# Kernel tuning notes

Measured on AMD Instinct MI355X. Metric: run time of the kernel, lower is better.

## Reference

```python
import jax, jax.numpy as jnp
import numpy as np

N, E, E3, DIM = 25000, 50000, 40000, 64


def setup_inputs() -> dict:
    key = jax.random.key(0)
    ks = jax.random.split(key, 16)
    def g(k, shape, scale=0.1):
        return jax.random.normal(k, shape, jnp.float32) * scale
    return {
        "x": jax.random.normal(ks[0], (N, 8), jnp.float32),
        "edge_attr": jax.random.uniform(ks[1], (E, 19), dtype=jnp.float32),
        "edge_attr3": jax.random.uniform(ks[2], (E3, 8), dtype=jnp.float32),
        "edge_index": jax.random.randint(ks[3], (2, E), 0, N),
        "edge_index3": jax.random.randint(ks[4], (2, E3), 0, N),
        "W_node": g(ks[5], (8, DIM)), "b_node": jnp.zeros((DIM,), jnp.float32),
        "W_ea": g(ks[6], (19, 12)), "b_ea": jnp.zeros((12,), jnp.float32),
        "W_e1": g(ks[7], (12, 128)), "b_e1": jnp.zeros((128,), jnp.float32),
        "W_e2": g(ks[8], (128, DIM * DIM), 0.01), "b_e2": jnp.zeros((DIM * DIM,), jnp.float32),
        "conv_bias": jnp.zeros((DIM,), jnp.float32),
        "W_ih": g(ks[9], (3 * DIM, DIM)), "b_ih": jnp.zeros((3 * DIM,), jnp.float32),
        "W_hh": g(ks[10], (3 * DIM, DIM)), "b_hh": jnp.zeros((3 * DIM,), jnp.float32),
        "W_l1": g(ks[11], (DIM + 8, 128)), "b_l1": jnp.zeros((128,), jnp.float32),
        "W_l2": g(ks[12], (128, 1)), "b_l2": jnp.zeros((1,), jnp.float32),
    }


def _forward(x, edge_attr, edge_attr3,
             W_node, b_node, W_ea, b_ea, W_e1, b_e1, W_e2, b_e2, conv_bias,
             W_ih, b_ih, W_hh, b_hh, W_l1, b_l1, W_l2, b_l2,
             edge_index, edge_index3):
    dim = W_node.shape[1]
    n = x.shape[0]
    out = jax.nn.relu(x @ W_node + b_node)                      # [N, dim]
    ea = jax.nn.relu(edge_attr @ W_ea + b_ea)                   # [E, 12]
    # edge MLP -> per-edge dim x dim weight matrices (same for all 3 conv calls)
    Wedge = (jax.nn.relu(ea @ W_e1 + b_e1) @ W_e2 + b_e2).reshape(-1, dim, dim)  # [E, dim, dim]
    src, dst = edge_index[0], edge_index[1]
    ones = jnp.ones((src.shape[0],), x.dtype)
    cnt = jnp.maximum(jax.ops.segment_sum(ones, dst, num_segments=n), 1.0)  # [N]
    h = out
    for _ in range(3):
        msg = jnp.einsum('ed,edf->ef', out[src], Wedge)                     # per-edge GEMV
        agg = jax.ops.segment_sum(msg, dst, num_segments=n) / cnt[:, None]  # scatter-mean
        m = jax.nn.relu(agg + conv_bias)
        # single-step GRU (PyTorch gate order: r, z, n)
        gi = m @ W_ih.T + b_ih
        gh = h @ W_hh.T + b_hh
        ir, iz, inn = jnp.split(gi, 3, axis=-1)
        hr, hz, hn = jnp.split(gh, 3, axis=-1)
        r = jax.nn.sigmoid(ir + hr)
        z = jax.nn.sigmoid(iz + hz)
        ng = jnp.tanh(inn + r * hn)
        h = (1.0 - z) * ng + z * h
        out = h
    pair = (out[edge_index3[0]] + out[edge_index3[1]]) * 0.5    # mean over the 2 endpoints
    yhat = jnp.concatenate([pair, edge_attr3], axis=1)          # [E3, dim+8]
    yhat = jax.nn.relu(yhat @ W_l1 + b_l1) @ W_l2 + b_l2        # [E3, 1]
    return yhat[:, 0]


def reference(x, edge_attr, edge_attr3, edge_index, edge_index3,
              W_node, b_node, W_ea, b_ea, W_e1, b_e1, W_e2, b_e2, conv_bias,
              W_ih, b_ih, W_hh, b_hh, W_l1, b_l1, W_l2, b_l2):
    return _forward(x, edge_attr, edge_attr3,
                    W_node, b_node, W_ea, b_ea, W_e1, b_e1, W_e2, b_e2, conv_bias,
                    W_ih, b_ih, W_hh, b_hh, W_l1, b_l1, W_l2, b_l2,
                    edge_index, edge_index3)
```

## Files before the change

### kernel.cpp

```cpp
#include <hip/hip_runtime.h>

typedef unsigned short u16;
typedef unsigned int u32;
typedef __attribute__((ext_vector_type(8))) short short8v;
typedef __attribute__((ext_vector_type(4))) float float4v;

__device__ __forceinline__ float sigm(float x) { return 1.0f / (1.0f + __expf(-x)); }
__device__ __forceinline__ u16 f2bf(float f) {
  u32 u = __float_as_uint(f);
  u32 r = (u + 0x7fffu + ((u >> 16) & 1u)) >> 16;
  return (u16)r;
}
__device__ __forceinline__ float bf2f(u16 w) { return __uint_as_float(((u32)w) << 16); }

__global__ void k_zero_f(float* __restrict__ p, int n) {
  int i = blockIdx.x * blockDim.x + threadIdx.x;
  if (i < n) p[i] = 0.0f;
}
__global__ void k_zero_i(int* __restrict__ p, int n) {
  int i = blockIdx.x * blockDim.x + threadIdx.x;
  if (i < n) p[i] = 0;
}

__global__ void k_cnt(const int* __restrict__ dst, int* __restrict__ cnt, int E) {
  int e = blockIdx.x * blockDim.x + threadIdx.x;
  if (e < E) atomicAdd(&cnt[dst[e]], 1);
}

__global__ void k_node(const float* __restrict__ x, const float* __restrict__ Wn,
                       const float* __restrict__ bn, float* __restrict__ h, int N) {
  int tid = blockIdx.x * blockDim.x + threadIdx.x;
  if (tid >= N * 64) return;
  int n = tid >> 6, f = tid & 63;
  float acc = bn[f];
  for (int k = 0; k < 8; ++k) acc += x[(size_t)n * 8 + k] * Wn[k * 64 + f];
  h[tid] = fmaxf(acc, 0.0f);
}

__global__ __launch_bounds__(256) void k_edge_mlp(
    const float* __restrict__ ea_in, const float* __restrict__ Wea,
    const float* __restrict__ bea, const float* __restrict__ We1,
    const float* __restrict__ be1, u16* __restrict__ Ahi, int E) {
  __shared__ float att[2][19];
  __shared__ float ea[2][12];
  int half = threadIdx.x >> 7;
  int t = threadIdx.x & 127;
  int e = blockIdx.x * 2 + half;
  bool real = (e < E);
  int ee = real ? e : E - 1;
  if (t < 19) att[half][t] = ea_in[(size_t)ee * 19 + t];
  __syncthreads();
  if (t < 12) {
    float a = bea[t];
#pragma unroll
    for (int k = 0; k < 19; ++k) a += att[half][k] * Wea[k * 12 + t];
    ea[half][t] = fmaxf(a, 0.0f);
  }
  __syncthreads();
  float a = be1[t];
#pragma unroll
  for (int j = 0; j < 12; ++j) a += ea[half][j] * We1[j * 128 + t];
  if (real) Ahi[(size_t)e * 128 + t] = f2bf(fmaxf(a, 0.0f));
}

__global__ void k_pack_b(const float* __restrict__ W2, u16* __restrict__ Bph) {
  int tid = blockIdx.x * blockDim.x + threadIdx.x;
  if (tid >= 128 * 4096) return;
  int j = tid & 7;
  int lane = (tid >> 3) & 63;
  int nt = (tid >> 9) & 3;
  int ks = (tid >> 11) & 3;
  int d = tid >> 13;
  int c = lane & 15, q = lane >> 4;
  int k = ks * 32 + q * 8 + j;
  int n = d * 64 + nt * 16 + c;
  Bph[tid] = f2bf(W2[(size_t)k * 4096 + n]);
}

__global__ void k_prep_wtf(const float* __restrict__ Wih, const float* __restrict__ Whh,
                           u16* __restrict__ WpI, u16* __restrict__ WpH) {
  int tid = blockIdx.x * blockDim.x + threadIdx.x;
  if (tid >= 2 * 12288) return;
  int w = tid / 12288;
  int r = tid - w * 12288;
  int jj = r & 7;
  int lane = (r >> 3) & 63;
  int t = r >> 9;
  int nt = t % 12, ks = t / 12;
  int c = lane & 15, q = lane >> 4;
  int j = nt * 16 + c;
  int k = ks * 32 + q * 8 + jj;
  const float* W = w ? Whh : Wih;
  u16* Wp = w ? WpH : WpI;
  Wp[r] = f2bf(W[j * 64 + k]);
}

__global__ void k_prep_wl1(const float* __restrict__ Wl1, u16* __restrict__ Wp1) {
  int tid = blockIdx.x * blockDim.x + threadIdx.x;
  if (tid >= 3 * 8 * 64 * 8) return;
  int j = tid & 7;
  int lane = (tid >> 3) & 63;
  int nt = (tid >> 9) & 7;
  int ks = tid >> 12;
  int c = lane & 15, q = lane >> 4;
  int k = ks * 32 + q * 8 + j;
  int n = nt * 16 + c;
  Wp1[tid] = f2bf((k < 72) ? Wl1[k * 128 + n] : 0.0f);
}

__global__ __launch_bounds__(256, 2) void k_conv_fused(
    const u16* __restrict__ Ahi, const u16* __restrict__ Bph,
    const float* __restrict__ b2, const float* __restrict__ h,
    const int* __restrict__ src, const int* __restrict__ dst,
    float* __restrict__ agg, int E) {
  __shared__ __align__(16) u16 sAh[128 * 136];
  __shared__ __align__(16) float hs[128 * 36];
  __shared__ __align__(16) float sb2[2048];
  int m0 = blockIdx.x * 128;
  int d0 = blockIdx.y * 32;
  int tid = threadIdx.x;
#pragma unroll
  for (int p = 0; p < 8; ++p) {
    int slot = p * 256 + tid;
    int r = slot >> 4, s = slot & 15;
    int gr = m0 + r;
    if (gr >= E) gr = E - 1;
    *(uint4*)(&sAh[r * 136 + s * 8]) = *(const uint4*)(Ahi + (size_t)gr * 128 + s * 8);
  }
#pragma unroll
  for (int p = 0; p < 4; ++p) {
    int slot = p * 256 + tid;
    int r = slot >> 3, s = slot & 7;
    int ge = m0 + r;
    if (ge >= E) ge = E - 1;
    int sn = src[ge];
    *(float4*)(&hs[r * 36 + s * 4]) = *(const float4*)(h + (size_t)sn * 64 + d0 + s * 4);
  }
#pragma unroll
  for (int p = 0; p < 2; ++p) {
    int slot = p * 256 + tid;
    *(float4*)(&sb2[slot * 4]) = *(const float4*)(b2 + d0 * 64 + slot * 4);
  }
  __syncthreads();
  int wave = tid >> 6, lane = tid & 63;
  int c = lane & 15, q = lane >> 4;
  float msg[2][4][4];
#pragma unroll
  for (int mt = 0; mt < 2; ++mt)
#pragma unroll
    for (int nt = 0; nt < 4; ++nt)
#pragma unroll
      for (int r = 0; r < 4; ++r) msg[mt][nt][r] = 0.0f;

  short8v bufA[16], bufB[16];
  auto loadB = [&](int dd, short8v* buf) {
    const u16* bp = Bph + (size_t)dd * 8192 + lane * 8;
#pragma unroll
    for (int i = 0; i < 16; ++i) buf[i] = *(const short8v*)(bp + i * 512);
  };
  auto compute = [&](int dd, const short8v* buf) {
    int dl = dd - d0;
#pragma unroll
    for (int mt = 0; mt < 2; ++mt) {
      int arow = wave * 32 + mt * 16 + c;
      float4v acc[4];
#pragma unroll
      for (int nt = 0; nt < 4; ++nt) acc[nt] = (float4v){0.f, 0.f, 0.f, 0.f};
#pragma unroll
      for (int ks = 0; ks < 4; ++ks) {
        short8v ah = *(const short8v*)(&sAh[arow * 136 + ks * 32 + q * 8]);
#pragma unroll
        for (int nt = 0; nt < 4; ++nt)
          acc[nt] = __builtin_amdgcn_mfma_f32_16x16x32_bf16(ah, buf[ks * 4 + nt], acc[nt], 0, 0, 0);
      }
      float hd[4];
#pragma unroll
      for (int r = 0; r < 4; ++r)
        hd[r] = hs[(wave * 32 + mt * 16 + q * 4 + r) * 36 + dl];
#pragma unroll
      for (int nt = 0; nt < 4; ++nt) {
        float b2v = sb2[dl * 64 + nt * 16 + c];
#pragma unroll
        for (int r = 0; r < 4; ++r) msg[mt][nt][r] += hd[r] * (acc[nt][r] + b2v);
      }
    }
  };

  loadB(d0, bufA);
  for (int d = d0; d < d0 + 32; d += 2) {
    loadB(d + 1, bufB);
    compute(d, bufA);
    if (d + 2 < d0 + 32) loadB(d + 2, bufA);
    compute(d + 1, bufB);
  }
#pragma unroll
  for (int mt = 0; mt < 2; ++mt) {
#pragma unroll
    for (int r = 0; r < 4; ++r) {
      int e = m0 + wave * 32 + mt * 16 + q * 4 + r;
      if (e < E) {
        int dn = dst[e];
        float* ap = agg + (size_t)dn * 64 + c;
#pragma unroll
        for (int nt = 0; nt < 4; ++nt) atomicAdd(ap + nt * 16, msg[mt][nt][r]);
      }
    }
  }
}

__global__ __launch_bounds__(256, 2) void k_gru_mfma(
    float* __restrict__ agg, const int* __restrict__ cnt,
    const float* __restrict__ cb, const u16* __restrict__ WpI,
    const u16* __restrict__ WpH, const float* __restrict__ bih,
    const float* __restrict__ bhh, const float* __restrict__ hin,
    float* __restrict__ hout, int N) {
  __shared__ __align__(16) u16 sM[64 * 72];
  __shared__ __align__(16) u16 sH[64 * 72];
  __shared__ __align__(16) float sHf[64 * 68];
  int n0 = blockIdx.x * 64;
  int tid = threadIdx.x;
#pragma unroll
  for (int p = 0; p < 16; ++p) {
    int slot = p * 256 + tid;
    int n = slot >> 6, f = slot & 63;
    int gn = n0 + n;
    bool real = (gn < N);
    if (!real) gn = N - 1;
    float cf = fmaxf((float)cnt[gn], 1.0f);
    float av = agg[(size_t)gn * 64 + f];
    if (real) agg[(size_t)gn * 64 + f] = 0.0f;
    float m = fmaxf(av / cf + cb[f], 0.0f);
    float hv = hin[(size_t)gn * 64 + f];
    sM[n * 72 + f] = f2bf(m);
    sH[n * 72 + f] = f2bf(hv);
    sHf[n * 68 + f] = hv;
  }
  __syncthreads();
  int wave = tid >> 6, lane = tid & 63;
  int c = lane & 15, q = lane >> 4;
  short8v am[2], ah[2];
#pragma unroll
  for (int ks = 0; ks < 2; ++ks) {
    am[ks] = *(const short8v*)(&sM[(wave * 16 + c) * 72 + ks * 32 + q * 8]);
    ah[ks] = *(const short8v*)(&sH[(wave * 16 + c) * 72 + ks * 32 + q * 8]);
  }
  float4v accRZ[8], accN[4], accHN[4];
#pragma unroll
  for (int i = 0; i < 8; ++i) accRZ[i] = (float4v){0.f, 0.f, 0.f, 0.f};
#pragma unroll
  for (int i = 0; i < 4; ++i) {
    accN[i] = (float4v){0.f, 0.f, 0.f, 0.f};
    accHN[i] = (float4v){0.f, 0.f, 0.f, 0.f};
  }
#pragma unroll
  for (int ks = 0; ks < 2; ++ks) {
#pragma unroll
    for (int nt = 0; nt < 8; ++nt) {
      short8v bI = *(const short8v*)(WpI + ((size_t)(ks * 12 + nt) * 64 + lane) * 8);
      short8v bH = *(const short8v*)(WpH + ((size_t)(ks * 12 + nt) * 64 + lane) * 8);
      accRZ[nt] = __builtin_amdgcn_mfma_f32_16x16x32_bf16(am[ks], bI, accRZ[nt], 0, 0, 0);
      accRZ[nt] = __builtin_amdgcn_mfma_f32_16x16x32_bf16(ah[ks], bH, accRZ[nt], 0, 0, 0);
    }
#pragma unroll
    for (int nt = 0; nt < 4; ++nt) {
      short8v bI = *(const short8v*)(WpI + ((size_t)(ks * 12 + 8 + nt) * 64 + lane) * 8);
      short8v bH = *(const short8v*)(WpH + ((size_t)(ks * 12 + 8 + nt) * 64 + lane) * 8);
      accN[nt] = __builtin_amdgcn_mfma_f32_16x16x32_bf16(am[ks], bI, accN[nt], 0, 0, 0);
      accHN[nt] = __builtin_amdgcn_mfma_f32_16x16x32_bf16(ah[ks], bH, accHN[nt], 0, 0, 0);
    }
  }
#pragma unroll
  for (int nt = 0; nt < 4; ++nt) {
    int f = nt * 16 + c;
    float brz_r = bih[f] + bhh[f];
    float brz_z = bih[64 + f] + bhh[64 + f];
    float bin = bih[128 + f];
    float bhn = bhh[128 + f];
#pragma unroll
    for (int r = 0; r < 4; ++r) {
      int nl = wave * 16 + q * 4 + r;
      int gn = n0 + nl;
      float rr = sigm(accRZ[nt][r] + brz_r);
      float zz = sigm(accRZ[nt + 4][r] + brz_z);
      float ng = tanhf(accN[nt][r] + bin + rr * (accHN[nt][r] + bhn));
      float hv = sHf[nl * 68 + f];
      if (gn < N) hout[(size_t)gn * 64 + f] = (1.0f - zz) * ng + zz * hv;
    }
  }
}

__global__ __launch_bounds__(256) void k_final_mfma(
    const float* __restrict__ h, const float* __restrict__ ea3,
    const int* __restrict__ idx3, const u16* __restrict__ Wp1,
    const float* __restrict__ bl1, const float* __restrict__ Wl2,
    const float* __restrict__ bl2, float* __restrict__ out, int E3) {
  __shared__ __align__(16) u16 sF[64 * 104];
  int e0 = blockIdx.x * 64;
  int tid = threadIdx.x;
  {
    int er = tid >> 2;
    int part = tid & 3;
    int ge = e0 + er;
    int gc = (ge < E3) ? ge : E3 - 1;
    int a = idx3[gc], b = idx3[E3 + gc];
    for (int kk = part * 24; kk < part * 24 + 24; ++kk) {
      float v;
      if (kk < 64) v = 0.5f * (h[(size_t)a * 64 + kk] + h[(size_t)b * 64 + kk]);
      else if (kk < 72) v = ea3[(size_t)gc * 8 + (kk - 64)];
      else v = 0.0f;
      sF[er * 104 + kk] = f2bf(v);
    }
  }
  __syncthreads();
  int wave = tid >> 6, lane = tid & 63;
  int c = lane & 15, q = lane >> 4;
  float4v acc[8];
#pragma unroll
  for (int nt = 0; nt < 8; ++nt) acc[nt] = (float4v){0.f, 0.f, 0.f, 0.f};
#pragma unroll
  for (int ks = 0; ks < 3; ++ks) {
    short8v af = *(const short8v*)(&sF[(wave * 16 + c) * 104 + ks * 32 + q * 8]);
#pragma unroll
    for (int nt = 0; nt < 8; ++nt) {
      short8v bf = *(const short8v*)(Wp1 + ((size_t)(ks * 8 + nt) * 64 + lane) * 8);
      acc[nt] = __builtin_amdgcn_mfma_f32_16x16x32_bf16(af, bf, acc[nt], 0, 0, 0);
    }
  }
  float v[4] = {0.f, 0.f, 0.f, 0.f};
#pragma unroll
  for (int nt = 0; nt < 8; ++nt) {
    int n = nt * 16 + c;
    float b1 = bl1[n];
    float w2 = Wl2[n];
#pragma unroll
    for (int r = 0; r < 4; ++r) v[r] += fmaxf(acc[nt][r] + b1, 0.0f) * w2;
  }
#pragma unroll
  for (int off = 1; off < 16; off <<= 1) {
#pragma unroll
    for (int r = 0; r < 4; ++r) v[r] += __shfl_xor(v[r], off);
  }
  if (c == 0) {
    float b2v = bl2[0];
#pragma unroll
    for (int r = 0; r < 4; ++r) {
      int e = e0 + wave * 16 + q * 4 + r;
      if (e < E3) out[e] = v[r] + b2v;
    }
  }
}

extern "C" void kernel_launch(void* const* d_in, const int* in_sizes, int n_in,
                              void* d_out, int out_size, void* d_ws, size_t ws_size,
                              hipStream_t stream) {
  const float* x          = (const float*)d_in[0];
  const float* edge_attr  = (const float*)d_in[1];
  const float* edge_attr3 = (const float*)d_in[2];
  const int*   edge_index = (const int*)d_in[3];
  const int*   edge_index3= (const int*)d_in[4];
  const float* W_node = (const float*)d_in[5];
  const float* b_node = (const float*)d_in[6];
  const float* W_ea   = (const float*)d_in[7];
  const float* b_ea   = (const float*)d_in[8];
  const float* W_e1   = (const float*)d_in[9];
  const float* b_e1   = (const float*)d_in[10];
  const float* W_e2   = (const float*)d_in[11];
  const float* b_e2   = (const float*)d_in[12];
  const float* conv_bias = (const float*)d_in[13];
  const float* W_ih   = (const float*)d_in[14];
  const float* b_ih   = (const float*)d_in[15];
  const float* W_hh   = (const float*)d_in[16];
  const float* b_hh   = (const float*)d_in[17];
  const float* W_l1   = (const float*)d_in[18];
  const float* b_l1   = (const float*)d_in[19];
  const float* W_l2   = (const float*)d_in[20];
  const float* b_l2   = (const float*)d_in[21];

  int N  = in_sizes[0] / 8;
  int E  = in_sizes[1] / 19;
  int E3 = in_sizes[2] / 8;

  char* p = (char*)d_ws;
  auto carve = [&](size_t bytes) -> void* {
    char* q = p;
    p += (bytes + 255) & ~(size_t)255;
    return (void*)q;
  };
  float* hA   = (float*)carve((size_t)N * 64 * 4);
  float* hB   = (float*)carve((size_t)N * 64 * 4);
  float* agg  = (float*)carve((size_t)N * 64 * 4);
  int*   cnt  = (int*)carve((size_t)N * 4);
  u16*   Ahi  = (u16*)carve((size_t)E * 128 * 2);
  u16*   Bph  = (u16*)carve((size_t)128 * 4096 * 2);
  u16*   WpI  = (u16*)carve(12288 * 2);
  u16*   WpH  = (u16*)carve(12288 * 2);
  u16*   Wp1  = (u16*)carve(12288 * 2);

  const int* src = edge_index;
  const int* dst = edge_index + E;

  k_zero_i<<<(N + 255) / 256, 256, 0, stream>>>(cnt, N);
  k_cnt<<<(E + 255) / 256, 256, 0, stream>>>(dst, cnt, E);
  k_node<<<((size_t)N * 64 + 255) / 256, 256, 0, stream>>>(x, W_node, b_node, hA, N);
  k_edge_mlp<<<(E + 1) / 2, 256, 0, stream>>>(edge_attr, W_ea, b_ea, W_e1, b_e1, Ahi, E);
  k_pack_b<<<(128 * 4096 + 255) / 256, 256, 0, stream>>>(W_e2, Bph);
  k_prep_wtf<<<(2 * 12288 + 255) / 256, 256, 0, stream>>>(W_ih, W_hh, WpI, WpH);
  k_prep_wl1<<<(12288 + 255) / 256, 256, 0, stream>>>(W_l1, Wp1);
  k_zero_f<<<((size_t)N * 64 + 255) / 256, 256, 0, stream>>>(agg, N * 64);

  float* hcur = hA;
  float* hnxt = hB;
  dim3 gconv((E + 127) / 128, 2);
  int ngru = (N + 63) / 64;
  for (int it = 0; it < 3; ++it) {
    k_conv_fused<<<gconv, 256, 0, stream>>>(Ahi, Bph, b_e2, hcur, src, dst, agg, E);
    k_gru_mfma<<<ngru, 256, 0, stream>>>(agg, cnt, conv_bias, WpI, WpH,
                                         b_ih, b_hh, hcur, hnxt, N);
    float* tmp = hcur; hcur = hnxt; hnxt = tmp;
  }
  k_final_mfma<<<(E3 + 63) / 64, 256, 0, stream>>>(hcur, edge_attr3, edge_index3, Wp1,
                                                   b_l1, W_l2, b_l2, (float*)d_out, E3);
}
```

Measured before the change: 450.3 us.

## Merge setup kernels, split conv over four d-chunks, coalesce final gather

Eight small setup kernels become two launches: one for zeroing and weight packing, one for edge counts, the node MLP and the edge MLP. The conv kernel now covers 16 d-columns per block instead of 32, with a y-grid of 4, to get more parallelism and smaller shared memory. In exchange it doubles the A-tile reloads and the atomic scatter traffic. The final kernel's gather now has each thread read one feature column, so h loads are coalesced instead of strided per thread.

```diff
diff --git a/kernel.cpp b/kernel.cpp
--- a/kernel.cpp
+++ b/kernel.cpp
@@ -13,39 +13,91 @@
 }
 __device__ __forceinline__ float bf2f(u16 w) { return __uint_as_float(((u32)w) << 16); }
 
-__global__ void k_zero_f(float* __restrict__ p, int n) {
-  int i = blockIdx.x * blockDim.x + threadIdx.x;
-  if (i < n) p[i] = 0.0f;
-}
-__global__ void k_zero_i(int* __restrict__ p, int n) {
-  int i = blockIdx.x * blockDim.x + threadIdx.x;
-  if (i < n) p[i] = 0;
-}
-
-__global__ void k_cnt(const int* __restrict__ dst, int* __restrict__ cnt, int E) {
-  int e = blockIdx.x * blockDim.x + threadIdx.x;
-  if (e < E) atomicAdd(&cnt[dst[e]], 1);
-}
-
-__global__ void k_node(const float* __restrict__ x, const float* __restrict__ Wn,
-                       const float* __restrict__ bn, float* __restrict__ h, int N) {
-  int tid = blockIdx.x * blockDim.x + threadIdx.x;
-  if (tid >= N * 64) return;
-  int n = tid >> 6, f = tid & 63;
-  float acc = bn[f];
-  for (int k = 0; k < 8; ++k) acc += x[(size_t)n * 8 + k] * Wn[k * 64 + f];
-  h[tid] = fmaxf(acc, 0.0f);
-}
-
-__global__ __launch_bounds__(256) void k_edge_mlp(
+__global__ void k_prep_all(const float* __restrict__ W2, const float* __restrict__ Wih,
+                           const float* __restrict__ Whh, const float* __restrict__ Wl1,
+                           u16* __restrict__ Bph, u16* __restrict__ WpI,
+                           u16* __restrict__ WpH, u16* __restrict__ Wp1,
+                           int* __restrict__ cnt, float* __restrict__ agg, int N) {
+  long long i = (long long)blockIdx.x * blockDim.x + threadIdx.x;
+  long long r0 = N;
+  long long r1 = r0 + (long long)N * 64;
+  long long r2 = r1 + 524288;
+  long long r3 = r2 + 24576;
+  long long r4 = r3 + 12288;
+  if (i < r0) {
+    cnt[i] = 0;
+  } else if (i < r1) {
+    agg[i - r0] = 0.0f;
+  } else if (i < r2) {
+    int tid = (int)(i - r1);
+    int j = tid & 7;
+    int lane = (tid >> 3) & 63;
+    int nt = (tid >> 9) & 3;
+    int ks = (tid >> 11) & 3;
+    int d = tid >> 13;
+    int c = lane & 15, q = lane >> 4;
+    int k = ks * 32 + q * 8 + j;
+    int n = d * 64 + nt * 16 + c;
+    Bph[tid] = f2bf(W2[(size_t)k * 4096 + n]);
+  } else if (i < r3) {
+    int tid = (int)(i - r2);
+    int w = tid / 12288;
+    int r = tid - w * 12288;
+    int jj = r & 7;
+    int lane = (r >> 3) & 63;
+    int t = r >> 9;
+    int nt = t % 12, ks = t / 12;
+    int c = lane & 15, q = lane >> 4;
+    int j = nt * 16 + c;
+    int k = ks * 32 + q * 8 + jj;
+    const float* W = w ? Whh : Wih;
+    u16* Wp = w ? WpH : WpI;
+    Wp[r] = f2bf(W[j * 64 + k]);
+  } else if (i < r4) {
+    int tid = (int)(i - r3);
+    int j = tid & 7;
+    int lane = (tid >> 3) & 63;
+    int nt = (tid >> 9) & 7;
+    int ks = tid >> 12;
+    int c = lane & 15, q = lane >> 4;
+    int k = ks * 32 + q * 8 + j;
+    int n = nt * 16 + c;
+    Wp1[tid] = f2bf((k < 72) ? Wl1[k * 128 + n] : 0.0f);
+  }
+}
+
+__global__ __launch_bounds__(256) void k_inputs(
+    const int* __restrict__ dst, int* __restrict__ cnt,
+    const float* __restrict__ x, const float* __restrict__ Wn,
+    const float* __restrict__ bn, float* __restrict__ h,
     const float* __restrict__ ea_in, const float* __restrict__ Wea,
     const float* __restrict__ bea, const float* __restrict__ We1,
-    const float* __restrict__ be1, u16* __restrict__ Ahi, int E) {
+    const float* __restrict__ be1, u16* __restrict__ Ahi, int N, int E) {
+  int nb_cnt = (E + 255) / 256;
+  int nb_node = (N * 64 + 255) / 256;
+  int b = blockIdx.x;
+  if (b < nb_cnt) {
+    int e = b * 256 + threadIdx.x;
+    if (e < E) atomicAdd(&cnt[dst[e]], 1);
+    return;
+  }
+  b -= nb_cnt;
+  if (b < nb_node) {
+    int tid = b * 256 + threadIdx.x;
+    if (tid < N * 64) {
+      int n = tid >> 6, f = tid & 63;
+      float acc = bn[f];
+      for (int k = 0; k < 8; ++k) acc += x[(size_t)n * 8 + k] * Wn[k * 64 + f];
+      h[tid] = fmaxf(acc, 0.0f);
+    }
+    return;
+  }
+  b -= nb_node;
   __shared__ float att[2][19];
   __shared__ float ea[2][12];
   int half = threadIdx.x >> 7;
   int t = threadIdx.x & 127;
-  int e = blockIdx.x * 2 + half;
+  int e = b * 2 + half;
   bool real = (e < E);
   int ee = real ? e : E - 1;
   if (t < 19) att[half][t] = ea_in[(size_t)ee * 19 + t];
@@ -63,61 +115,16 @@
   if (real) Ahi[(size_t)e * 128 + t] = f2bf(fmaxf(a, 0.0f));
 }
 
-__global__ void k_pack_b(const float* __restrict__ W2, u16* __restrict__ Bph) {
-  int tid = blockIdx.x * blockDim.x + threadIdx.x;
-  if (tid >= 128 * 4096) return;
-  int j = tid & 7;
-  int lane = (tid >> 3) & 63;
-  int nt = (tid >> 9) & 3;
-  int ks = (tid >> 11) & 3;
-  int d = tid >> 13;
-  int c = lane & 15, q = lane >> 4;
-  int k = ks * 32 + q * 8 + j;
-  int n = d * 64 + nt * 16 + c;
-  Bph[tid] = f2bf(W2[(size_t)k * 4096 + n]);
-}
-
-__global__ void k_prep_wtf(const float* __restrict__ Wih, const float* __restrict__ Whh,
-                           u16* __restrict__ WpI, u16* __restrict__ WpH) {
-  int tid = blockIdx.x * blockDim.x + threadIdx.x;
-  if (tid >= 2 * 12288) return;
-  int w = tid / 12288;
-  int r = tid - w * 12288;
-  int jj = r & 7;
-  int lane = (r >> 3) & 63;
-  int t = r >> 9;
-  int nt = t % 12, ks = t / 12;
-  int c = lane & 15, q = lane >> 4;
-  int j = nt * 16 + c;
-  int k = ks * 32 + q * 8 + jj;
-  const float* W = w ? Whh : Wih;
-  u16* Wp = w ? WpH : WpI;
-  Wp[r] = f2bf(W[j * 64 + k]);
-}
-
-__global__ void k_prep_wl1(const float* __restrict__ Wl1, u16* __restrict__ Wp1) {
-  int tid = blockIdx.x * blockDim.x + threadIdx.x;
-  if (tid >= 3 * 8 * 64 * 8) return;
-  int j = tid & 7;
-  int lane = (tid >> 3) & 63;
-  int nt = (tid >> 9) & 7;
-  int ks = tid >> 12;
-  int c = lane & 15, q = lane >> 4;
-  int k = ks * 32 + q * 8 + j;
-  int n = nt * 16 + c;
-  Wp1[tid] = f2bf((k < 72) ? Wl1[k * 128 + n] : 0.0f);
-}
-
 __global__ __launch_bounds__(256, 2) void k_conv_fused(
     const u16* __restrict__ Ahi, const u16* __restrict__ Bph,
     const float* __restrict__ b2, const float* __restrict__ h,
     const int* __restrict__ src, const int* __restrict__ dst,
     float* __restrict__ agg, int E) {
   __shared__ __align__(16) u16 sAh[128 * 136];
-  __shared__ __align__(16) float hs[128 * 36];
-  __shared__ __align__(16) float sb2[2048];
+  __shared__ __align__(16) float hs[128 * 20];
+  __shared__ __align__(16) float sb2[1024];
   int m0 = blockIdx.x * 128;
-  int d0 = blockIdx.y * 32;
+  int d0 = blockIdx.y * 16;
   int tid = threadIdx.x;
 #pragma unroll
   for (int p = 0; p < 8; ++p) {
@@ -128,17 +135,16 @@
     *(uint4*)(&sAh[r * 136 + s * 8]) = *(const uint4*)(Ahi + (size_t)gr * 128 + s * 8);
   }
 #pragma unroll
-  for (int p = 0; p < 4; ++p) {
+  for (int p = 0; p < 2; ++p) {
     int slot = p * 256 + tid;
-    int r = slot >> 3, s = slot & 7;
+    int r = slot >> 2, s = slot & 3;
     int ge = m0 + r;
     if (ge >= E) ge = E - 1;
     int sn = src[ge];
-    *(float4*)(&hs[r * 36 + s * 4]) = *(const float4*)(h + (size_t)sn * 64 + d0 + s * 4);
-  }
-#pragma unroll
-  for (int p = 0; p < 2; ++p) {
-    int slot = p * 256 + tid;
+    *(float4*)(&hs[r * 20 + s * 4]) = *(const float4*)(h + (size_t)sn * 64 + d0 + s * 4);
+  }
+  {
+    int slot = tid;
     *(float4*)(&sb2[slot * 4]) = *(const float4*)(b2 + d0 * 64 + slot * 4);
   }
   __syncthreads();
@@ -176,7 +182,7 @@
       float hd[4];
 #pragma unroll
       for (int r = 0; r < 4; ++r)
-        hd[r] = hs[(wave * 32 + mt * 16 + q * 4 + r) * 36 + dl];
+        hd[r] = hs[(wave * 32 + mt * 16 + q * 4 + r) * 20 + dl];
 #pragma unroll
       for (int nt = 0; nt < 4; ++nt) {
         float b2v = sb2[dl * 64 + nt * 16 + c];
@@ -187,10 +193,10 @@
   };
 
   loadB(d0, bufA);
-  for (int d = d0; d < d0 + 32; d += 2) {
+  for (int d = d0; d < d0 + 16; d += 2) {
     loadB(d + 1, bufB);
     compute(d, bufA);
-    if (d + 2 < d0 + 32) loadB(d + 2, bufA);
+    if (d + 2 < d0 + 16) loadB(d + 2, bufA);
     compute(d + 1, bufB);
   }
 #pragma unroll
@@ -297,19 +303,24 @@
   __shared__ __align__(16) u16 sF[64 * 104];
   int e0 = blockIdx.x * 64;
   int tid = threadIdx.x;
-  {
-    int er = tid >> 2;
-    int part = tid & 3;
+#pragma unroll
+  for (int p = 0; p < 16; ++p) {
+    int er = p * 4 + (tid >> 6);
+    int kk = tid & 63;
     int ge = e0 + er;
     int gc = (ge < E3) ? ge : E3 - 1;
     int a = idx3[gc], b = idx3[E3 + gc];
-    for (int kk = part * 24; kk < part * 24 + 24; ++kk) {
-      float v;
-      if (kk < 64) v = 0.5f * (h[(size_t)a * 64 + kk] + h[(size_t)b * 64 + kk]);
-      else if (kk < 72) v = ea3[(size_t)gc * 8 + (kk - 64)];
-      else v = 0.0f;
-      sF[er * 104 + kk] = f2bf(v);
-    }
+    sF[er * 104 + kk] = f2bf(0.5f * (h[(size_t)a * 64 + kk] + h[(size_t)b * 64 + kk]));
+  }
+#pragma unroll
+  for (int p = 0; p < 8; ++p) {
+    int slot = p * 256 + tid;
+    int er = slot >> 5;
+    int kk = 64 + (slot & 31);
+    int ge = e0 + er;
+    int gc = (ge < E3) ? ge : E3 - 1;
+    float v = (kk < 72) ? ea3[(size_t)gc * 8 + (kk - 64)] : 0.0f;
+    sF[er * 104 + kk] = f2bf(v);
   }
   __syncthreads();
   int wave = tid >> 6, lane = tid & 63;
@@ -399,18 +410,18 @@
   const int* src = edge_index;
   const int* dst = edge_index + E;
 
-  k_zero_i<<<(N + 255) / 256, 256, 0, stream>>>(cnt, N);
-  k_cnt<<<(E + 255) / 256, 256, 0, stream>>>(dst, cnt, E);
-  k_node<<<((size_t)N * 64 + 255) / 256, 256, 0, stream>>>(x, W_node, b_node, hA, N);
-  k_edge_mlp<<<(E + 1) / 2, 256, 0, stream>>>(edge_attr, W_ea, b_ea, W_e1, b_e1, Ahi, E);
-  k_pack_b<<<(128 * 4096 + 255) / 256, 256, 0, stream>>>(W_e2, Bph);
-  k_prep_wtf<<<(2 * 12288 + 255) / 256, 256, 0, stream>>>(W_ih, W_hh, WpI, WpH);
-  k_prep_wl1<<<(12288 + 255) / 256, 256, 0, stream>>>(W_l1, Wp1);
-  k_zero_f<<<((size_t)N * 64 + 255) / 256, 256, 0, stream>>>(agg, N * 64);
+  long long prep_tot = (long long)N + (long long)N * 64 + 524288 + 24576 + 12288;
+  k_prep_all<<<(unsigned)((prep_tot + 255) / 256), 256, 0, stream>>>(
+      W_e2, W_ih, W_hh, W_l1, Bph, WpI, WpH, Wp1, cnt, agg, N);
+  int nb_cnt = (E + 255) / 256;
+  int nb_node = (N * 64 + 255) / 256;
+  int nb_edge = (E + 1) / 2;
+  k_inputs<<<nb_cnt + nb_node + nb_edge, 256, 0, stream>>>(
+      dst, cnt, x, W_node, b_node, hA, edge_attr, W_ea, b_ea, W_e1, b_e1, Ahi, N, E);
 
   float* hcur = hA;
   float* hnxt = hB;
-  dim3 gconv((E + 127) / 128, 2);
+  dim3 gconv((E + 127) / 128, 4);
   int ngru = (N + 63) / 64;
   for (int it = 0; it < 3; ++it) {
     k_conv_fused<<<gconv, 256, 0, stream>>>(Ahi, Bph, b_e2, hcur, src, dst, agg, E);
```

Result: no change. 453.8 us (+0.8%).
